# Kernel tuning notes

Measured on AMD Instinct MI355X. Metric: run time of the kernel, lower is better.

## Reference

```python
import jax, jax.numpy as jnp
import numpy as np

# Static config (matches init_kwargs)
VOCAB, EMBED, HIDDEN = 32000, 256, 512
SLOTS, MEM_DIM, HEADS, TOPK = 1024, 64, 4, 8
B, T = 16, 128
# beta_read/beta_write are learned scalars but the torch forward detaches them
# via .item(); treat as constants (|beta| + 1e-6 with beta init ~1.0).
BETA_R = 1.0 + 1e-6
BETA_W = 1.0 + 1e-6
EPS = 1e-8


def setup_inputs() -> dict:
    key = jax.random.key(0)
    ks = jax.random.split(key, 16)
    s = 0.02
    HD = HEADS * MEM_DIM
    return {
        "input_seq": jax.random.randint(ks[0], (B, T), 0, VOCAB),
        "E": jax.random.normal(ks[1], (VOCAB, EMBED), jnp.float32) * s,
        "W_ih": jax.random.normal(ks[2], (4 * HIDDEN, EMBED + MEM_DIM), jnp.float32) * s,
        "W_hh": jax.random.normal(ks[3], (4 * HIDDEN, HIDDEN), jnp.float32) * s,
        "b_ih": jnp.zeros((4 * HIDDEN,), jnp.float32),
        "b_hh": jnp.zeros((4 * HIDDEN,), jnp.float32),
        "W_out": jax.random.normal(ks[4], (HIDDEN, VOCAB), jnp.float32) * s,
        "b_out": jnp.zeros((VOCAB,), jnp.float32),
        "W_rk": jax.random.normal(ks[5], (HIDDEN, HD), jnp.float32) * s,
        "b_rk": jnp.zeros((HD,), jnp.float32),
        "W_wk": jax.random.normal(ks[6], (HIDDEN, HD), jnp.float32) * s,
        "b_wk": jnp.zeros((HD,), jnp.float32),
        "W_wv": jax.random.normal(ks[7], (HIDDEN, HD), jnp.float32) * s,
        "b_wv": jnp.zeros((HD,), jnp.float32),
        "W_er": jax.random.normal(ks[8], (HIDDEN, HD), jnp.float32) * s,
        "b_er": jnp.zeros((HD,), jnp.float32),
    }


def _address(memory, keys, beta):
    # memory: [B,S,D], keys: [B,H,D] -> sparse (top-k) content weights [B,H,S]
    mem_n = memory / (jnp.linalg.norm(memory, axis=-1, keepdims=True) + EPS)
    key_n = keys / (jnp.linalg.norm(keys, axis=-1, keepdims=True) + EPS)
    scores = beta * jnp.einsum("bhd,bsd->bhs", key_n, mem_n)
    vals, idx = jax.lax.top_k(scores, TOPK)           # [B,H,K]
    sm = jax.nn.softmax(vals, axis=-1)                # softmax over top-k only
    w = jnp.zeros_like(scores)
    b_ix = jnp.arange(scores.shape[0])[:, None, None]
    h_ix = jnp.arange(HEADS)[None, :, None]
    return w.at[b_ix, h_ix, idx].set(sm)              # [B,H,S]


def reference(input_seq, E, W_ih, W_hh, b_ih, b_hh, W_out, b_out,
              W_rk, b_rk, W_wk, b_wk, W_wv, b_wv, W_er, b_er):
    Bq = input_seq.shape[0]
    memory0 = jnp.full((Bq, SLOTS, MEM_DIM), 1e-6, jnp.float32)
    h0 = jnp.zeros((Bq, HIDDEN), jnp.float32)
    c0 = jnp.zeros((Bq, HIDDEN), jnp.float32)
    r0 = jnp.zeros((Bq, MEM_DIM), jnp.float32)

    def step(carry, x_t):
        memory, h, c, read_vec = carry
        emb = E[x_t]                                          # [B,embed]
        inp = jnp.concatenate([emb, read_vec], axis=-1)
        gates = inp @ W_ih.T + b_ih + h @ W_hh.T + b_hh       # [B,4H]
        i, f, g, o = jnp.split(gates, 4, axis=-1)             # torch LSTM order
        c = jax.nn.sigmoid(f) * c + jax.nn.sigmoid(i) * jnp.tanh(g)
        h = jax.nn.sigmoid(o) * jnp.tanh(c)
        logits = h @ W_out + b_out                            # [B,V]
        rk = (h @ W_rk + b_rk).reshape(Bq, HEADS, MEM_DIM)
        wk = (h @ W_wk + b_wk).reshape(Bq, HEADS, MEM_DIM)
        wv = (h @ W_wv + b_wv).reshape(Bq, HEADS, MEM_DIM)
        er = jax.nn.sigmoid(h @ W_er + b_er).reshape(Bq, HEADS, MEM_DIM)
        # content-addressed top-k read
        rw = _address(memory, rk, BETA_R)                     # [B,H,S]
        read_vec = jnp.einsum("bhs,bsd->bhd", rw, memory).mean(axis=1)
        # erase + add write
        ww = _address(memory, wk, BETA_W)                     # [B,H,S]
        keep = jnp.prod(1.0 - ww[..., None] * er[:, :, None, :], axis=1)
        add = jnp.einsum("bhs,bhd->bsd", ww, wv)
        memory = memory * keep + add
        return (memory, h, c, read_vec), logits

    _, logits_seq = jax.lax.scan(step, (memory0, h0, c0, r0), input_seq.T)
    return jnp.transpose(logits_seq, (1, 0, 2))               # [B,T,V]
```

## Files before the change

kernel.cpp:

```cpp
#include <hip/hip_runtime.h>
#include <hip/hip_bf16.h>
#include <stdint.h>

typedef unsigned int uint;
typedef unsigned short ushort;
typedef unsigned long long u64;
typedef __attribute__((ext_vector_type(8))) short s8v;
typedef __attribute__((ext_vector_type(4))) float f4v;

#define T_STEPS 128
#define BQ 16
#define HID 512
#define NSLOT 1024
#define MD 64
#define VOCAB 32000
#define BETA 1.000001f
#define EPSN 1e-8f

#define NWK 128
#define NBT 16

#define LF_FH(b)  ((b)*32)
#define LF_FP(w)  ((16+(w))*32)
#define LF_FC(w)  ((48+(w))*32)
#define LF_FW(b)  ((176+(b))*32)
#define LF_FG(w)  ((192+(w))*32)
#define NLINES    320

#define AL4(dst, p) asm volatile("global_load_dwordx4 %0, %1, off sc0 sc1" : "=v"(dst) : "v"(p))
#define ALF(dst, p) asm volatile("global_load_dword %0, %1, off sc0 sc1" : "=v"(dst) : "v"(p))
#define AWAIT() do { asm volatile("s_waitcnt vmcnt(0)" ::: "memory"); __builtin_amdgcn_sched_barrier(0); } while(0)
#define DRAIN() asm volatile("s_waitcnt vmcnt(0)" ::: "memory")

__device__ __forceinline__ float sigm(float x){ return 1.f/(1.f+expf(-x)); }
__device__ __forceinline__ void astoref(float* p, float v){
  __hip_atomic_store(p, v, __ATOMIC_RELAXED, __HIP_MEMORY_SCOPE_AGENT);
}
__device__ __forceinline__ void astoreu32(uint* p, uint v){
  __hip_atomic_store(p, v, __ATOMIC_RELAXED, __HIP_MEMORY_SCOPE_AGENT);
}
__device__ __forceinline__ void astoreu64(u64* p, u64 v){
  __hip_atomic_store(p, v, __ATOMIC_RELAXED, __HIP_MEMORY_SCOPE_AGENT);
}
__device__ __forceinline__ u64 aloadu64(const u64* p){
  return __hip_atomic_load((u64*)p, __ATOMIC_RELAXED, __HIP_MEMORY_SCOPE_AGENT);
}
__device__ __forceinline__ uint aloadu32(const uint* p){
  return __hip_atomic_load((uint*)p, __ATOMIC_RELAXED, __HIP_MEMORY_SCOPE_AGENT);
}
__device__ __forceinline__ void poll1(const uint* p, uint gen){
  while (aloadu32(p) < gen) __builtin_amdgcn_s_sleep(2);
}

__device__ __forceinline__ u64 packsc(float v, int slot){
  uint u = __float_as_uint(v);
  u = (u & 0x80000000u) ? ~u : (u | 0x80000000u);
  return ((u64)u << 10) | (u64)(1023 - slot);
}
__device__ __forceinline__ float unpackval(u64 p){
  uint u = (uint)(p >> 10);
  uint bits = (u & 0x80000000u) ? (u & 0x7fffffffu) : ~u;
  return __uint_as_float(bits);
}
__device__ __forceinline__ int unpackslot(u64 p){ return 1023 - (int)(p & 1023u); }

__device__ __forceinline__ ushort f2bf(float x){
  __hip_bfloat16 h = __float2bfloat16(x);
  return *(ushort*)&h;
}
__device__ __forceinline__ float bf2f(ushort u){
  __hip_bfloat16 h; *(ushort*)&h = u;
  return __bfloat162float(h);
}

#define L_MEM  0
#define L_NRM  8704
#define L_HS   8832
#define L_KEY  17088
#define L_KNRM 17600
#define L_SC   17608
#define L_WV   18632
#define L_ER   18888
#define L_WL   19144
#define L_TOT  19208

__global__ __launch_bounds__(256) void prep_emb(const float* __restrict__ E,
                                                const int* __restrict__ seq,
                                                float* __restrict__ EMB){
  int m = blockIdx.x, t = m >> 4, b = m & 15;
  int x = seq[b*T_STEPS + t];
  EMB[(size_t)m*256 + threadIdx.x] = E[(size_t)x*256 + threadIdx.x];
}

__global__ __launch_bounds__(256) void gemm_emb(const float* __restrict__ A,
                                                const float* __restrict__ W_ih,
                                                const float* __restrict__ b_ih,
                                                const float* __restrict__ b_hh,
                                                float* __restrict__ C){
  __shared__ __align__(16) float As[16*68];
  __shared__ __align__(16) float Bs[16*68];
  int mt = blockIdx.x & 31, nt = blockIdx.x >> 5;
  int m0 = mt*64, n0 = nt*64;
  int tx = threadIdx.x & 15, ty = threadIdx.x >> 4;
  float acc[4][4] = {};
  for (int k0 = 0; k0 < 256; k0 += 16){
    int mm = threadIdx.x >> 2, kq = (threadIdx.x & 3)*4;
    float4 a = *(const float4*)(A + (size_t)(m0+mm)*256 + k0 + kq);
    As[(kq+0)*68+mm]=a.x; As[(kq+1)*68+mm]=a.y; As[(kq+2)*68+mm]=a.z; As[(kq+3)*68+mm]=a.w;
    int pp = n0 + mm;
    int r = (pp & 3)*512 + (pp >> 2);
    float4 bv = *(const float4*)(W_ih + (size_t)r*320 + k0 + kq);
    Bs[(kq+0)*68+mm]=bv.x; Bs[(kq+1)*68+mm]=bv.y; Bs[(kq+2)*68+mm]=bv.z; Bs[(kq+3)*68+mm]=bv.w;
    __syncthreads();
    #pragma unroll
    for (int kk = 0; kk < 16; ++kk){
      float4 av = *(const float4*)(As + kk*68 + ty*4);
      float4 bb = *(const float4*)(Bs + kk*68 + tx*4);
      float aa[4] = {av.x,av.y,av.z,av.w};
      float bv2[4] = {bb.x,bb.y,bb.z,bb.w};
      #pragma unroll
      for (int i = 0; i < 4; ++i)
        #pragma unroll
        for (int j = 0; j < 4; ++j)
          acc[i][j] = fmaf(aa[i], bv2[j], acc[i][j]);
    }
    __syncthreads();
  }
  #pragma unroll
  for (int i = 0; i < 4; ++i){
    int m = m0 + ty*4 + i;
    #pragma unroll
    for (int j = 0; j < 4; ++j){
      int pp = n0 + tx*4 + j;
      int r = (pp & 3)*512 + (pp >> 2);
      C[(size_t)m*2048 + pp] = acc[i][j] + b_ih[r] + b_hh[r];
    }
  }
}

__global__ __launch_bounds__(256) void make_wrvT(const float* __restrict__ W_ih,
                                                 float* __restrict__ WT){
  int idx = blockIdx.x*256 + threadIdx.x;
  int k = idx >> 11, p = idx & 2047;
  int r = (p & 3)*512 + (p >> 2);
  WT[idx] = W_ih[(size_t)r*320 + 256 + k];
}

__global__ __launch_bounds__(256) void split_BT(const float* __restrict__ W,
                                                ushort* __restrict__ BThi,
                                                ushort* __restrict__ BTlo){
  __shared__ float tl[32][33];
  int kt = blockIdx.x & 15, nt = blockIdx.x >> 4;
  int k0 = kt*32, n0 = nt*32;
  int tx = threadIdx.x & 31, ty = threadIdx.x >> 5;
  #pragma unroll
  for (int i = 0; i < 4; ++i)
    tl[ty + i*8][tx] = W[(size_t)(k0 + ty + i*8)*VOCAB + n0 + tx];
  __syncthreads();
  #pragma unroll
  for (int i = 0; i < 4; ++i){
    float x = tl[tx][ty + i*8];
    ushort hi = f2bf(x);
    ushort lo = f2bf(x - bf2f(hi));
    size_t o = (size_t)(n0 + ty + i*8)*512 + k0 + tx;
    BThi[o] = hi; BTlo[o] = lo;
  }
}

__global__ __launch_bounds__(256) void split_A(const float* __restrict__ H,
                                               ushort* __restrict__ Ahi,
                                               ushort* __restrict__ Alo){
  int idx = blockIdx.x*256 + threadIdx.x;
  float x = H[idx];
  ushort hi = f2bf(x);
  Ahi[idx] = hi;
  Alo[idx] = f2bf(x - bf2f(hi));
}

__global__ __launch_bounds__(256) void recur_kernel(
    const float* __restrict__ W_hh, const float* __restrict__ WT,
    const float* __restrict__ W_rk, const float* __restrict__ b_rk,
    const float* __restrict__ W_wk, const float* __restrict__ b_wk,
    const float* __restrict__ W_wv, const float* __restrict__ b_wv,
    const float* __restrict__ W_er, const float* __restrict__ b_er,
    const float* __restrict__ G_emb, float* __restrict__ H_all,
    float* __restrict__ H_pub, float* __restrict__ mem_g,
    float* __restrict__ projpub, float* __restrict__ gatespub,
    u64* __restrict__ cand, u64* __restrict__ wlist,
    uint* __restrict__ arrv)
{
  __shared__ __align__(16) float smem[L_TOT];
  const int tid = threadIdx.x;
  const int wg  = blockIdx.x;

  if (wg < NWK){
    float* mem_s  = smem + L_MEM;
    float* nrm_s  = smem + L_NRM;
    float* hs     = smem + L_HS;
    float* key_s  = smem + L_KEY;
    float* knrm_s = smem + L_KNRM;
    float* sc_s   = smem + L_SC;
    float* wv_s   = smem + L_WV;
    float* er_s   = smem + L_ER;
    u64*   wl_s   = (u64*)(smem + L_WL);

    const int b_s = wg >> 3, rg = wg & 7, s0 = rg*128;
    const int gb = tid >> 4, gc = tid & 15;
    const int pcol = wg*16 + gc;
    const int rrow = (pcol & 3)*512 + (pcol >> 2);
    float* mslice_g = mem_g + ((size_t)b_s*NSLOT + s0)*MD;
    const float* W1 = (wg < 16) ? W_rk : W_wk;
    const float* B1 = (wg < 16) ? b_rk : b_wk;
    const float* W2 = (wg < 16) ? W_wv : W_er;
    const float* B2 = (wg < 16) ? b_wv : b_er;
    const int cc = (wg & 15)*16 + gc;
    const float pb1 = (wg < 32) ? B1[cc] : 0.f;
    const float pb2 = (wg < 32) ? B2[cc] : 0.f;

    for (int i = tid; i < 128*MD; i += 256){
      mem_s[(i >> 6)*68 + (i & 63)] = 1e-6f;
      astoref(mslice_g + i, 1e-6f);
    }
    __syncthreads();
    {
      int s = tid >> 1, half = tid & 1;
      const float4* mp = (const float4*)(mem_s + s*68 + half*32);
      float sum = 0.f;
      #pragma unroll
      for (int q = 0; q < 8; ++q){
        float4 v = mp[q];
        sum = fmaf(v.x,v.x,sum); sum = fmaf(v.y,v.y,sum);
        sum = fmaf(v.z,v.z,sum); sum = fmaf(v.w,v.w,sum);
      }
      sum += __shfl_xor(sum, 1);
      if (half == 0) nrm_s[s] = sqrtf(sum) + EPSN;
    }
    __syncthreads();

    #pragma clang loop unroll(disable)
    for (int t = 0; t < T_STEPS-1; ++t){
      const int par = t & 1, parp = par ^ 1;
      if (t > 0){
        if (tid == 0) poll1(arrv + LF_FW(b_s), (uint)t);
        __syncthreads();
        if (tid < 32) wl_s[tid] = aloadu64(wlist + (size_t)b_s*32 + tid);
        if (tid < 64){
          float4 v; AL4(v, (const float4*)(projpub + (size_t)parp*BQ*1024 + (size_t)b_s*1024 + 512) + tid);
          AWAIT();
          *(float4*)(wv_s + tid*4) = v;
        } else if (tid < 128){
          int i = tid - 64;
          float4 v; AL4(v, (const float4*)(projpub + (size_t)parp*BQ*1024 + (size_t)b_s*1024 + 768) + i);
          AWAIT();
          *(float4*)(er_s + i*4) = v;
        }
        __syncthreads();
        if (tid < 64){
          const int d = tid;
          #pragma unroll 1
          for (int e = 0; e < 32; ++e){
            u64 w64 = wl_s[e];
            int sl = (int)(w64 & 0xffffffffu);
            if (sl >= s0 && sl < s0+128){
              float w = __uint_as_float((uint)(w64 >> 32));
              mem_s[(sl-s0)*68 + d] *= (1.f - w*er_s[(e >> 3)*64 + d]);
            }
          }
          #pragma unroll 1
          for (int e = 0; e < 32; ++e){
            u64 w64 = wl_s[e];
            int sl = (int)(w64 & 0xffffffffu);
            if (sl >= s0 && sl < s0+128){
              float w = __uint_as_float((uint)(w64 >> 32));
              mem_s[(sl-s0)*68 + d] += w*wv_s[(e >> 3)*64 + d];
            }
          }
          #pragma unroll 1
          for (int e = 0; e < 32; ++e){
            u64 w64 = wl_s[e];
            int sl = (int)(w64 & 0xffffffffu);
            if (sl >= s0 && sl < s0+128)
              astoref(mslice_g + (sl-s0)*MD + d, mem_s[(sl-s0)*68 + d]);
          }
        }
        __syncthreads();
        {
          int s = tid >> 1, half = tid & 1;
          const float4* mp = (const float4*)(mem_s + s*68 + half*32);
          float sum = 0.f;
          #pragma unroll
          for (int q = 0; q < 8; ++q){
            float4 v = mp[q];
            sum = fmaf(v.x,v.x,sum); sum = fmaf(v.y,v.y,sum);
            sum = fmaf(v.z,v.z,sum); sum = fmaf(v.w,v.w,sum);
          }
          sum += __shfl_xor(sum, 1);
          if (half == 0) nrm_s[s] = sqrtf(sum) + EPSN;
        }
      }
      if (tid < 16) poll1(arrv + LF_FH(tid), (uint)(t+1));
      __syncthreads();
      {
        float4 v0,v1,v2,v3,v4,v5,v6,v7;
        const float4* hp = (const float4*)H_pub;
        AL4(v0, hp + tid);        AL4(v1, hp + tid + 256);
        AL4(v2, hp + tid + 512);  AL4(v3, hp + tid + 768);
        AL4(v4, hp + tid + 1024); AL4(v5, hp + tid + 1280);
        AL4(v6, hp + tid + 1536); AL4(v7, hp + tid + 1792);
        AWAIT();
        int i;
        i = tid;        *(float4*)(hs + (i>>7)*516 + (i&127)*4) = v0;
        i = tid + 256;  *(float4*)(hs + (i>>7)*516 + (i&127)*4) = v1;
        i = tid + 512;  *(float4*)(hs + (i>>7)*516 + (i&127)*4) = v2;
        i = tid + 768;  *(float4*)(hs + (i>>7)*516 + (i&127)*4) = v3;
        i = tid + 1024; *(float4*)(hs + (i>>7)*516 + (i&127)*4) = v4;
        i = tid + 1280; *(float4*)(hs + (i>>7)*516 + (i&127)*4) = v5;
        i = tid + 1536; *(float4*)(hs + (i>>7)*516 + (i&127)*4) = v6;
        i = tid + 1792; *(float4*)(hs + (i>>7)*516 + (i&127)*4) = v7;
      }
      __syncthreads();
      if (wg < 32){
        float a0=0.f,a1=0.f,b0=0.f,b1=0.f;
        const float* hp = hs + gb*516;
        const float* w1 = W1 + cc;
        const float* w2 = W2 + cc;
        #pragma unroll 4
        for (int k = 0; k < 512; k += 2){
          float h0 = hp[k], h1 = hp[k+1];
          a0 = fmaf(h0, w1[(size_t)k*256], a0);
          b0 = fmaf(h0, w2[(size_t)k*256], b0);
          a1 = fmaf(h1, w1[(size_t)(k+1)*256], a1);
          b1 = fmaf(h1, w2[(size_t)(k+1)*256], b1);
        }
        float v1 = a0 + a1 + pb1;
        float v2 = b0 + b1 + pb2;
        if (wg >= 16) v2 = sigm(v2);
        astoref(projpub + (size_t)par*BQ*1024 + (size_t)gb*1024 + wg*16 + gc, v1);
        astoref(projpub + (size_t)par*BQ*1024 + (size_t)gb*1024 + 512 + wg*16 + gc, v2);
      }
      DRAIN();
      __syncthreads();
      if (wg < 32 && tid == 0) astoreu32(arrv + LF_FP(wg), (uint)(t+1));
      if (tid < 32) poll1(arrv + LF_FP(tid), (uint)(t+1));
      __syncthreads();
      if (tid < 128){
        float4 kv; AL4(kv, (const float4*)(projpub + (size_t)par*BQ*1024 + (size_t)b_s*1024) + tid);
        AWAIT();
        *(float4*)(key_s + tid*4) = kv;
      }
      __syncthreads();
      if (tid < 8){
        const float4* kp = (const float4*)(key_s + tid*MD);
        float sum = 0.f;
        #pragma unroll
        for (int q = 0; q < 16; ++q){
          float4 v = kp[q];
          sum = fmaf(v.x,v.x,sum); sum = fmaf(v.y,v.y,sum);
          sum = fmaf(v.z,v.z,sum); sum = fmaf(v.w,v.w,sum);
        }
        knrm_s[tid] = sqrtf(sum) + EPSN;
      }
      __syncthreads();
      {
        int s = tid >> 1, kh = tid & 1;
        const float4* mp = (const float4*)(mem_s + s*68);
        float rnm = 1.f / nrm_s[s];
        float acc4[4] = {0.f,0.f,0.f,0.f};
        #pragma unroll
        for (int q = 0; q < 16; ++q){
          float4 m = mp[q];
          #pragma unroll
          for (int kk = 0; kk < 4; ++kk){
            float4 k4 = *(const float4*)(key_s + (kh*4+kk)*MD + q*4);
            acc4[kk] = fmaf(m.x,k4.x,acc4[kk]); acc4[kk] = fmaf(m.y,k4.y,acc4[kk]);
            acc4[kk] = fmaf(m.z,k4.z,acc4[kk]); acc4[kk] = fmaf(m.w,k4.w,acc4[kk]);
          }
        }
        #pragma unroll
        for (int kk = 0; kk < 4; ++kk){
          int key = kh*4 + kk;
          sc_s[key*128 + s] = BETA * acc4[kk] * rnm / knrm_s[key];
        }
      }
      __syncthreads();
      {
        int wid = tid >> 6, lane = tid & 63;
        #pragma unroll
        for (int kk = 0; kk < 2; ++kk){
          int key = wid*2 + kk;
          u64 p0 = packsc(sc_s[key*128 + lane],      s0 + lane);
          u64 p1 = packsc(sc_s[key*128 + 64 + lane], s0 + 64 + lane);
          #pragma unroll
          for (int r = 0; r < 8; ++r){
            u64 m = p0 > p1 ? p0 : p1;
            #pragma unroll
            for (int o = 32; o; o >>= 1){ u64 q = __shfl_xor(m, o); if (q > m) m = q; }
            if (p0 == m) p0 = 0; else if (p1 == m) p1 = 0;
            if (lane == 0) astoreu64(cand + (((size_t)b_s*8 + key)*8 + rg)*8 + r, m);
          }
        }
      }
      DRAIN();
      __syncthreads();
      if (tid == 0) astoreu32(arrv + LF_FC(wg), (uint)(t+1));
      {
        float a0 = G_emb[(size_t)((t+1)*BQ + gb)*2048 + pcol];
        float a1 = 0.f, a2 = 0.f, a3 = 0.f;
        const float4* wh = (const float4*)(W_hh + (size_t)rrow*HID);
        const float4* xv = (const float4*)(hs + gb*516);
        #pragma unroll 2
        for (int k = 0; k < 128; k += 4){
          float4 w, x;
          w=wh[k+0]; x=xv[k+0]; a0=fmaf(w.x,x.x,a0); a0=fmaf(w.y,x.y,a0); a0=fmaf(w.z,x.z,a0); a0=fmaf(w.w,x.w,a0);
          w=wh[k+1]; x=xv[k+1]; a1=fmaf(w.x,x.x,a1); a1=fmaf(w.y,x.y,a1); a1=fmaf(w.z,x.z,a1); a1=fmaf(w.w,x.w,a1);
          w=wh[k+2]; x=xv[k+2]; a2=fmaf(w.x,x.x,a2); a2=fmaf(w.y,x.y,a2); a2=fmaf(w.z,x.z,a2); a2=fmaf(w.w,x.w,a2);
          w=wh[k+3]; x=xv[k+3]; a3=fmaf(w.x,x.x,a3); a3=fmaf(w.y,x.y,a3); a3=fmaf(w.z,x.z,a3); a3=fmaf(w.w,x.w,a3);
        }
        astoref(gatespub + (size_t)gb*2048 + pcol, (a0+a1)+(a2+a3));
      }
      DRAIN();
      __syncthreads();
      if (tid == 0) astoreu32(arrv + LF_FG(wg), (uint)(t+1));
    }
  } else {
    const int b = wg - NWK;
    float* rv_st = smem;
    float* rv_s  = smem + 256;
    float* gl    = smem + 320;
    float c0, c1;
    {
      float4 gA = *(const float4*)(G_emb + (size_t)b*2048 + tid*8);
      float4 gB = *(const float4*)(G_emb + (size_t)b*2048 + tid*8 + 4);
      c0 = sigm(gA.x)*tanhf(gA.z);
      float h0v = sigm(gA.w)*tanhf(c0);
      c1 = sigm(gB.x)*tanhf(gB.z);
      float h1v = sigm(gB.w)*tanhf(c1);
      astoref(H_pub + (size_t)b*HID + tid*2,     h0v);
      astoref(H_pub + (size_t)b*HID + tid*2 + 1, h1v);
      H_all[(size_t)b*HID + tid*2]     = h0v;
      H_all[(size_t)b*HID + tid*2 + 1] = h1v;
    }
    DRAIN();
    __syncthreads();
    if (tid == 0) astoreu32(arrv + LF_FH(b), 1u);

    #pragma clang loop unroll(disable)
    for (int t = 0; t < T_STEPS-1; ++t){
      if (tid < 8) poll1(arrv + LF_FC(b*8 + tid), (uint)(t+1));
      __syncthreads();
      {
        int wid = tid >> 6, lane = tid & 63;
        #pragma unroll
        for (int kk = 0; kk < 2; ++kk){
          int key = wid*2 + kk;
          u64 pv = aloadu64(cand + (((size_t)b*8 + key)*8 + (lane >> 3))*8 + (lane & 7));
          u64 sel = 0;
          #pragma unroll
          for (int r = 0; r < 8; ++r){
            u64 m = pv;
            #pragma unroll
            for (int o = 32; o; o >>= 1){ u64 q = __shfl_xor(m, o); if (q > m) m = q; }
            if (pv == m) pv = 0;
            if (lane == r) sel = m;
          }
          float val = unpackval(sel);
          int slot = unpackslot(sel);
          float vmax = __shfl(val, 0);
          float e = (lane < 8) ? expf(val - vmax) : 0.f;
          float ssum = e;
          #pragma unroll
          for (int o = 32; o; o >>= 1) ssum += __shfl_xor(ssum, o);
          float w = e / ssum;
          if (key < 4){
            int sls[8];
            #pragma unroll
            for (int i = 0; i < 8; ++i) sls[i] = __shfl(slot, i);
            float mv[8];
            #pragma unroll
            for (int i = 0; i < 8; ++i)
              ALF(mv[i], mem_g + ((size_t)b*NSLOT + sls[i])*MD + lane);
            AWAIT();
            float acc = 0.f;
            #pragma unroll
            for (int i = 0; i < 8; ++i) acc = fmaf(__shfl(w, i), mv[i], acc);
            rv_st[key*64 + lane] = acc;
          } else if (lane < 8){
            astoreu64(wlist + (size_t)b*32 + (key-4)*8 + lane,
                      ((u64)__float_as_uint(w) << 32) | (u64)(uint)slot);
          }
        }
      }
      DRAIN();
      __syncthreads();
      if (tid < 64)
        rv_s[tid] = 0.25f*(rv_st[tid] + rv_st[64+tid] + rv_st[128+tid] + rv_st[192+tid]);
      if (tid == 0) astoreu32(arrv + LF_FW(b), (uint)(t+1));
      if (tid < 128) poll1(arrv + LF_FG(tid), (uint)(t+1));
      __syncthreads();
      {
        float g8[8];
        #pragma unroll
        for (int q = 0; q < 8; ++q)
          ALF(g8[q], gatespub + (size_t)b*2048 + tid + 256*q);
        AWAIT();
        #pragma unroll 2
        for (int d = 0; d < 64; ++d){
          float r = rv_s[d];
          const float* wrow = WT + (size_t)d*2048 + tid;
          #pragma unroll
          for (int q = 0; q < 8; ++q)
            g8[q] = fmaf(r, wrow[256*q], g8[q]);
        }
        #pragma unroll
        for (int q = 0; q < 8; ++q) gl[tid + 256*q] = g8[q];
      }
      __syncthreads();
      {
        float gi0 = gl[tid*8+0], gf0 = gl[tid*8+1], gg0 = gl[tid*8+2], go0 = gl[tid*8+3];
        float gi1 = gl[tid*8+4], gf1 = gl[tid*8+5], gg1 = gl[tid*8+6], go1 = gl[tid*8+7];
        c0 = sigm(gf0)*c0 + sigm(gi0)*tanhf(gg0);
        float h0v = sigm(go0)*tanhf(c0);
        c1 = sigm(gf1)*c1 + sigm(gi1)*tanhf(gg1);
        float h1v = sigm(go1)*tanhf(c1);
        astoref(H_pub + (size_t)b*HID + tid*2,     h0v);
        astoref(H_pub + (size_t)b*HID + tid*2 + 1, h1v);
        H_all[(size_t)((t+1)*BQ + b)*HID + tid*2]     = h0v;
        H_all[(size_t)((t+1)*BQ + b)*HID + tid*2 + 1] = h1v;
      }
      DRAIN();
      __syncthreads();
      if (tid == 0) astoreu32(arrv + LF_FH(b), (uint)(t+2));
    }
  }
}

#define GM_NT 250
__global__ __launch_bounds__(256) void gemm_mfma(
    const ushort* __restrict__ Ahi, const ushort* __restrict__ Alo,
    const ushort* __restrict__ BThi, const ushort* __restrict__ BTlo,
    const float* __restrict__ bias, float* __restrict__ C)
{
  __shared__ __align__(16) ushort ldsu[4*128*40];
  const int tid = threadIdx.x;
  int mt = blockIdx.x / GM_NT, nt = blockIdx.x - mt*GM_NT;
  int m0 = mt*128, n0 = nt*128;
  const int wv = tid >> 6, lane = tid & 63;
  const int wm = (wv & 1)*64, wn = (wv >> 1)*64;
  const int fr = lane & 15, kh = (lane >> 4)*8;

  f4v acc[4][4];
  #pragma unroll
  for (int i = 0; i < 4; ++i)
    #pragma unroll
    for (int j = 0; j < 4; ++j)
      acc[i][j] = (f4v){0.f,0.f,0.f,0.f};

  const int sr = tid & 127, sel = tid >> 7;
  const ushort* srcA = (sel ? Alo : Ahi) + (size_t)(m0 + sr)*512;
  const ushort* srcB = (sel ? BTlo : BThi) + (size_t)(n0 + sr)*512;
  ushort* dstA = ldsu + (size_t)sel*5120 + sr*40;
  ushort* dstB = ldsu + (size_t)(2+sel)*5120 + sr*40;

  for (int ks = 0; ks < 16; ++ks){
    const int k0 = ks*32;
    __syncthreads();
    {
      uint4 a0 = *(const uint4*)(srcA + k0);
      uint4 a1 = *(const uint4*)(srcA + k0 + 8);
      uint4 a2 = *(const uint4*)(srcA + k0 + 16);
      uint4 a3 = *(const uint4*)(srcA + k0 + 24);
      uint4 b0 = *(const uint4*)(srcB + k0);
      uint4 b1 = *(const uint4*)(srcB + k0 + 8);
      uint4 b2 = *(const uint4*)(srcB + k0 + 16);
      uint4 b3 = *(const uint4*)(srcB + k0 + 24);
      *(uint4*)(dstA +  0) = a0; *(uint4*)(dstA +  8) = a1;
      *(uint4*)(dstA + 16) = a2; *(uint4*)(dstA + 24) = a3;
      *(uint4*)(dstB +  0) = b0; *(uint4*)(dstB +  8) = b1;
      *(uint4*)(dstB + 16) = b2; *(uint4*)(dstB + 24) = b3;
    }
    __syncthreads();
    s8v ah[4], al[4], bh[4], bl[4];
    #pragma unroll
    for (int mi = 0; mi < 4; ++mi){
      ah[mi] = *(const s8v*)(ldsu + 0*5120 + (wm + mi*16 + fr)*40 + kh);
      al[mi] = *(const s8v*)(ldsu + 1*5120 + (wm + mi*16 + fr)*40 + kh);
    }
    #pragma unroll
    for (int ni = 0; ni < 4; ++ni){
      bh[ni] = *(const s8v*)(ldsu + 2*5120 + (wn + ni*16 + fr)*40 + kh);
      bl[ni] = *(const s8v*)(ldsu + 3*5120 + (wn + ni*16 + fr)*40 + kh);
    }
    #pragma unroll
    for (int mi = 0; mi < 4; ++mi)
      #pragma unroll
      for (int ni = 0; ni < 4; ++ni){
        acc[mi][ni] = __builtin_amdgcn_mfma_f32_16x16x32_bf16(ah[mi], bh[ni], acc[mi][ni], 0, 0, 0);
        acc[mi][ni] = __builtin_amdgcn_mfma_f32_16x16x32_bf16(ah[mi], bl[ni], acc[mi][ni], 0, 0, 0);
        acc[mi][ni] = __builtin_amdgcn_mfma_f32_16x16x32_bf16(al[mi], bh[ni], acc[mi][ni], 0, 0, 0);
        acc[mi][ni] = __builtin_amdgcn_mfma_f32_16x16x32_bf16(al[mi], bl[ni], acc[mi][ni], 0, 0, 0);
      }
  }
  #pragma unroll
  for (int ni = 0; ni < 4; ++ni){
    int col = n0 + wn + ni*16 + fr;
    float bz = bias[col];
    #pragma unroll
    for (int mi = 0; mi < 4; ++mi){
      #pragma unroll
      for (int j = 0; j < 4; ++j){
        int row = m0 + wm + mi*16 + (lane >> 4)*4 + j;
        C[((size_t)(row & 15)*T_STEPS + (row >> 4))*VOCAB + col] = acc[mi][ni][j] + bz;
      }
    }
  }
}

__global__ __launch_bounds__(256) void gemm_out(const float* __restrict__ A,
                                                const float* __restrict__ Bmat,
                                                const float* __restrict__ bias,
                                                float* __restrict__ C){
  __shared__ __align__(16) float As[16*132];
  __shared__ __align__(16) float Bs[16*64];
  int mt = blockIdx.x & 15, nt = blockIdx.x >> 4;
  int m0 = mt*128, n0 = nt*64;
  int tx = threadIdx.x & 15, ty = threadIdx.x >> 4;
  float acc[8][4] = {};
  for (int k0 = 0; k0 < 512; k0 += 16){
    int mm = threadIdx.x >> 1, kq = (threadIdx.x & 1)*8;
    float4 a0 = *(const float4*)(A + (size_t)(m0+mm)*512 + k0 + kq);
    float4 a1 = *(const float4*)(A + (size_t)(m0+mm)*512 + k0 + kq + 4);
    As[(kq+0)*132+mm]=a0.x; As[(kq+1)*132+mm]=a0.y; As[(kq+2)*132+mm]=a0.z; As[(kq+3)*132+mm]=a0.w;
    As[(kq+4)*132+mm]=a1.x; As[(kq+5)*132+mm]=a1.y; As[(kq+6)*132+mm]=a1.z; As[(kq+7)*132+mm]=a1.w;
    int kk2 = threadIdx.x >> 4, nq = (threadIdx.x & 15)*4;
    *(float4*)(Bs + kk2*64 + nq) = *(const float4*)(Bmat + (size_t)(k0+kk2)*VOCAB + n0 + nq);
    __syncthreads();
    #pragma unroll
    for (int kk = 0; kk < 16; ++kk){
      float4 x0 = *(const float4*)(As + kk*132 + ty*8);
      float4 x1 = *(const float4*)(As + kk*132 + ty*8 + 4);
      float4 bv = *(const float4*)(Bs + kk*64 + tx*4);
      float aa[8] = {x0.x,x0.y,x0.z,x0.w,x1.x,x1.y,x1.z,x1.w};
      float bb[4] = {bv.x,bv.y,bv.z,bv.w};
      #pragma unroll
      for (int i = 0; i < 8; ++i)
        #pragma unroll
        for (int j = 0; j < 4; ++j)
          acc[i][j] = fmaf(aa[i], bb[j], acc[i][j]);
    }
    __syncthreads();
  }
  #pragma unroll
  for (int i = 0; i < 8; ++i){
    int m = m0 + ty*8 + i;
    int bq = m & 15, tt = m >> 4;
    float* crow = C + ((size_t)bq*T_STEPS + tt)*VOCAB + n0 + tx*4;
    #pragma unroll
    for (int j = 0; j < 4; ++j) crow[j] = acc[i][j] + bias[n0 + tx*4 + j];
  }
}

extern "C" void kernel_launch(void* const* d_in, const int* in_sizes, int n_in,
                              void* d_out, int out_size, void* d_ws, size_t ws_size,
                              hipStream_t stream){
  const int*   seq   = (const int*)d_in[0];
  const float* E     = (const float*)d_in[1];
  const float* W_ih  = (const float*)d_in[2];
  const float* W_hh  = (const float*)d_in[3];
  const float* b_ih  = (const float*)d_in[4];
  const float* b_hh  = (const float*)d_in[5];
  const float* W_out = (const float*)d_in[6];
  const float* b_out = (const float*)d_in[7];
  const float* W_rk  = (const float*)d_in[8];
  const float* b_rk  = (const float*)d_in[9];
  const float* W_wk  = (const float*)d_in[10];
  const float* b_wk  = (const float*)d_in[11];
  const float* W_wv  = (const float*)d_in[12];
  const float* b_wv  = (const float*)d_in[13];
  const float* W_er  = (const float*)d_in[14];
  const float* b_er  = (const float*)d_in[15];
  float* out = (float*)d_out;
  (void)in_sizes; (void)n_in; (void)out_size;

  char* ws = (char*)d_ws;
  size_t off = 0;
  auto alloc = [&](size_t bytes) -> void* {
    off = (off + 255) & ~(size_t)255;
    void* p = ws + off;
    off += bytes;
    return p;
  };
  float* EMB      = (float*)alloc((size_t)2048*256*4);
  float* G_emb    = (float*)alloc((size_t)2048*2048*4);
  float* H_all    = (float*)alloc((size_t)2048*512*4);
  float* H_pub    = (float*)alloc((size_t)16*512*4);
  float* mem_g    = (float*)alloc((size_t)16*1024*64*4);
  float* projpub  = (float*)alloc((size_t)2*16*1024*4);
  float* gatespub = (float*)alloc((size_t)16*2048*4);
  u64*   cand     = (u64*)alloc((size_t)16*8*8*8*8);
  u64*   wlist    = (u64*)alloc((size_t)16*32*8);
  float* WT       = (float*)alloc((size_t)64*2048*4);
  uint*  arrv     = (uint*)alloc((size_t)NLINES*32*4);
  ushort* Ahi  = (ushort*)alloc((size_t)2048*512*2);
  ushort* Alo  = (ushort*)alloc((size_t)2048*512*2);
  ushort* BThi = (ushort*)alloc((size_t)VOCAB*512*2);
  ushort* BTlo = (ushort*)alloc((size_t)VOCAB*512*2);
  const bool use_mfma = (off <= ws_size);

  hipMemsetAsync(arrv, 0, (size_t)NLINES*32*4, stream);
  prep_emb<<<2048, 256, 0, stream>>>(E, seq, EMB);
  gemm_emb<<<1024, 256, 0, stream>>>(EMB, W_ih, b_ih, b_hh, G_emb);
  make_wrvT<<<512, 256, 0, stream>>>(W_ih, WT);
  if (use_mfma)
    split_BT<<<16000, 256, 0, stream>>>(W_out, BThi, BTlo);
  recur_kernel<<<NWK + NBT, 256, 0, stream>>>(
      W_hh, WT, W_rk, b_rk, W_wk, b_wk, W_wv, b_wv, W_er, b_er,
      G_emb, H_all, H_pub, mem_g, projpub, gatespub, cand, wlist, arrv);
  if (use_mfma){
    split_A<<<4096, 256, 0, stream>>>(H_all, Ahi, Alo);
    gemm_mfma<<<16*GM_NT, 256, 0, stream>>>(Ahi, Alo, BThi, BTlo, b_out, out);
  } else {
    gemm_out<<<16*500, 256, 0, stream>>>(H_all, W_out, b_out, out);
  }
}
```

Measured before the change: 6.386 ms.

## Overlap output-projection GEMM with recurrence via extra persistent workgroups

```diff
diff --git a/kernel.cpp b/kernel.cpp
--- a/kernel.cpp
+++ b/kernel.cpp
@@ -19,6 +19,8 @@
 
 #define NWK 128
 #define NBT 16
+#define NGEMM 256
+#define GM_NT 250
 
 #define LF_FH(b)  ((b)*32)
 #define LF_FP(w)  ((16+(w))*32)
@@ -50,6 +52,9 @@
 }
 __device__ __forceinline__ void poll1(const uint* p, uint gen){
   while (aloadu32(p) < gen) __builtin_amdgcn_s_sleep(2);
+}
+__device__ __forceinline__ void poll64(const uint* p, uint gen){
+  while (aloadu32(p) < gen) __builtin_amdgcn_s_sleep(64);
 }
 
 __device__ __forceinline__ u64 packsc(float v, int slot){
@@ -167,16 +172,6 @@
   }
 }
 
-__global__ __launch_bounds__(256) void split_A(const float* __restrict__ H,
-                                               ushort* __restrict__ Ahi,
-                                               ushort* __restrict__ Alo){
-  int idx = blockIdx.x*256 + threadIdx.x;
-  float x = H[idx];
-  ushort hi = f2bf(x);
-  Ahi[idx] = hi;
-  Alo[idx] = f2bf(x - bf2f(hi));
-}
-
 __global__ __launch_bounds__(256) void recur_kernel(
     const float* __restrict__ W_hh, const float* __restrict__ WT,
     const float* __restrict__ W_rk, const float* __restrict__ b_rk,
@@ -187,6 +182,8 @@
     float* __restrict__ H_pub, float* __restrict__ mem_g,
     float* __restrict__ projpub, float* __restrict__ gatespub,
     u64* __restrict__ cand, u64* __restrict__ wlist,
+    const ushort* __restrict__ BThi, const ushort* __restrict__ BTlo,
+    const float* __restrict__ b_out, float* __restrict__ C_out,
     uint* __restrict__ arrv)
 {
   __shared__ __align__(16) float smem[L_TOT];
@@ -422,7 +419,7 @@
       __syncthreads();
       if (tid == 0) astoreu32(arrv + LF_FG(wg), (uint)(t+1));
     }
-  } else {
+  } else if (wg < NWK + NBT){
     const int b = wg - NWK;
     float* rv_st = smem;
     float* rv_s  = smem + 256;
@@ -437,8 +434,8 @@
       float h1v = sigm(gB.w)*tanhf(c1);
       astoref(H_pub + (size_t)b*HID + tid*2,     h0v);
       astoref(H_pub + (size_t)b*HID + tid*2 + 1, h1v);
-      H_all[(size_t)b*HID + tid*2]     = h0v;
-      H_all[(size_t)b*HID + tid*2 + 1] = h1v;
+      astoref(H_all + (size_t)b*HID + tid*2,     h0v);
+      astoref(H_all + (size_t)b*HID + tid*2 + 1, h1v);
     }
     DRAIN();
     __syncthreads();
@@ -524,93 +521,98 @@
         float h1v = sigm(go1)*tanhf(c1);
         astoref(H_pub + (size_t)b*HID + tid*2,     h0v);
         astoref(H_pub + (size_t)b*HID + tid*2 + 1, h1v);
-        H_all[(size_t)((t+1)*BQ + b)*HID + tid*2]     = h0v;
-        H_all[(size_t)((t+1)*BQ + b)*HID + tid*2 + 1] = h1v;
+        astoref(H_all + (size_t)((t+1)*BQ + b)*HID + tid*2,     h0v);
+        astoref(H_all + (size_t)((t+1)*BQ + b)*HID + tid*2 + 1, h1v);
       }
       DRAIN();
       __syncthreads();
       if (tid == 0) astoreu32(arrv + LF_FH(b), (uint)(t+2));
     }
-  }
-}
-
-#define GM_NT 250
-__global__ __launch_bounds__(256) void gemm_mfma(
-    const ushort* __restrict__ Ahi, const ushort* __restrict__ Alo,
-    const ushort* __restrict__ BThi, const ushort* __restrict__ BTlo,
-    const float* __restrict__ bias, float* __restrict__ C)
-{
-  __shared__ __align__(16) ushort ldsu[4*128*40];
-  const int tid = threadIdx.x;
-  int mt = blockIdx.x / GM_NT, nt = blockIdx.x - mt*GM_NT;
-  int m0 = mt*128, n0 = nt*128;
-  const int wv = tid >> 6, lane = tid & 63;
-  const int wm = (wv & 1)*64, wn = (wv >> 1)*64;
-  const int fr = lane & 15, kh = (lane >> 4)*8;
-
-  f4v acc[4][4];
-  #pragma unroll
-  for (int i = 0; i < 4; ++i)
-    #pragma unroll
-    for (int j = 0; j < 4; ++j)
-      acc[i][j] = (f4v){0.f,0.f,0.f,0.f};
-
-  const int sr = tid & 127, sel = tid >> 7;
-  const ushort* srcA = (sel ? Alo : Ahi) + (size_t)(m0 + sr)*512;
-  const ushort* srcB = (sel ? BTlo : BThi) + (size_t)(n0 + sr)*512;
-  ushort* dstA = ldsu + (size_t)sel*5120 + sr*40;
-  ushort* dstB = ldsu + (size_t)(2+sel)*5120 + sr*40;
-
-  for (int ks = 0; ks < 16; ++ks){
-    const int k0 = ks*32;
-    __syncthreads();
-    {
-      uint4 a0 = *(const uint4*)(srcA + k0);
-      uint4 a1 = *(const uint4*)(srcA + k0 + 8);
-      uint4 a2 = *(const uint4*)(srcA + k0 + 16);
-      uint4 a3 = *(const uint4*)(srcA + k0 + 24);
-      uint4 b0 = *(const uint4*)(srcB + k0);
-      uint4 b1 = *(const uint4*)(srcB + k0 + 8);
-      uint4 b2 = *(const uint4*)(srcB + k0 + 16);
-      uint4 b3 = *(const uint4*)(srcB + k0 + 24);
-      *(uint4*)(dstA +  0) = a0; *(uint4*)(dstA +  8) = a1;
-      *(uint4*)(dstA + 16) = a2; *(uint4*)(dstA + 24) = a3;
-      *(uint4*)(dstB +  0) = b0; *(uint4*)(dstB +  8) = b1;
-      *(uint4*)(dstB + 16) = b2; *(uint4*)(dstB + 24) = b3;
-    }
-    __syncthreads();
-    s8v ah[4], al[4], bh[4], bl[4];
-    #pragma unroll
-    for (int mi = 0; mi < 4; ++mi){
-      ah[mi] = *(const s8v*)(ldsu + 0*5120 + (wm + mi*16 + fr)*40 + kh);
-      al[mi] = *(const s8v*)(ldsu + 1*5120 + (wm + mi*16 + fr)*40 + kh);
-    }
-    #pragma unroll
-    for (int ni = 0; ni < 4; ++ni){
-      bh[ni] = *(const s8v*)(ldsu + 2*5120 + (wn + ni*16 + fr)*40 + kh);
-      bl[ni] = *(const s8v*)(ldsu + 3*5120 + (wn + ni*16 + fr)*40 + kh);
-    }
-    #pragma unroll
-    for (int mi = 0; mi < 4; ++mi)
+  } else {
+    const int g = wg - (NWK + NBT);
+    ushort* ldsu = (ushort*)smem;
+    const int wv_ = tid >> 6, lane = tid & 63;
+    const int wm = (wv_ & 1)*64, wn = (wv_ >> 1)*64;
+    const int fr = lane & 15, kh = (lane >> 4)*8;
+    const int ar = tid >> 1, ahalf = tid & 1;
+    const int sr = tid & 127, selb = tid >> 7;
+
+    for (int tile = g; tile < 16*GM_NT; tile += NGEMM){
+      int mt = tile / GM_NT, nt = tile - mt*GM_NT;
+      int m0 = mt*128, n0 = nt*128;
+      uint need = (uint)(mt*8 + 8);
+      if (tid < 16) poll64(arrv + LF_FH(tid), need);
+      __syncthreads();
+      f4v acc[4][4];
+      #pragma unroll
+      for (int i = 0; i < 4; ++i)
+        #pragma unroll
+        for (int j = 0; j < 4; ++j)
+          acc[i][j] = (f4v){0.f,0.f,0.f,0.f};
+      const float* srcA = H_all + (size_t)(m0 + ar)*512 + ahalf*16;
+      const ushort* srcB = (selb ? BTlo : BThi) + (size_t)(n0 + sr)*512;
+      ushort* dstAh = ldsu + 0*5120 + ar*40 + ahalf*16;
+      ushort* dstAl = ldsu + 1*5120 + ar*40 + ahalf*16;
+      ushort* dstB  = ldsu + (size_t)(2+selb)*5120 + sr*40;
+      for (int ks = 0; ks < 16; ++ks){
+        const int k0 = ks*32;
+        __syncthreads();
+        float4 fa0, fa1, fa2, fa3;
+        AL4(fa0, (const float4*)(srcA + k0));
+        AL4(fa1, (const float4*)(srcA + k0 + 4));
+        AL4(fa2, (const float4*)(srcA + k0 + 8));
+        AL4(fa3, (const float4*)(srcA + k0 + 12));
+        uint4 b0 = *(const uint4*)(srcB + k0);
+        uint4 b1 = *(const uint4*)(srcB + k0 + 8);
+        uint4 b2 = *(const uint4*)(srcB + k0 + 16);
+        uint4 b3 = *(const uint4*)(srcB + k0 + 24);
+        AWAIT();
+        float fa[16] = {fa0.x,fa0.y,fa0.z,fa0.w, fa1.x,fa1.y,fa1.z,fa1.w,
+                        fa2.x,fa2.y,fa2.z,fa2.w, fa3.x,fa3.y,fa3.z,fa3.w};
+        #pragma unroll
+        for (int j = 0; j < 16; ++j){
+          ushort hi = f2bf(fa[j]);
+          dstAh[j] = hi;
+          dstAl[j] = f2bf(fa[j] - bf2f(hi));
+        }
+        *(uint4*)(dstB +  0) = b0; *(uint4*)(dstB +  8) = b1;
+        *(uint4*)(dstB + 16) = b2; *(uint4*)(dstB + 24) = b3;
+        __syncthreads();
+        s8v ah[4], al[4], bh[4], bl[4];
+        #pragma unroll
+        for (int mi = 0; mi < 4; ++mi){
+          ah[mi] = *(const s8v*)(ldsu + 0*5120 + (wm + mi*16 + fr)*40 + kh);
+          al[mi] = *(const s8v*)(ldsu + 1*5120 + (wm + mi*16 + fr)*40 + kh);
+        }
+        #pragma unroll
+        for (int ni = 0; ni < 4; ++ni){
+          bh[ni] = *(const s8v*)(ldsu + 2*5120 + (wn + ni*16 + fr)*40 + kh);
+          bl[ni] = *(const s8v*)(ldsu + 3*5120 + (wn + ni*16 + fr)*40 + kh);
+        }
+        #pragma unroll
+        for (int mi = 0; mi < 4; ++mi)
+          #pragma unroll
+          for (int ni = 0; ni < 4; ++ni){
+            acc[mi][ni] = __builtin_amdgcn_mfma_f32_16x16x32_bf16(ah[mi], bh[ni], acc[mi][ni], 0, 0, 0);
+            acc[mi][ni] = __builtin_amdgcn_mfma_f32_16x16x32_bf16(ah[mi], bl[ni], acc[mi][ni], 0, 0, 0);
+            acc[mi][ni] = __builtin_amdgcn_mfma_f32_16x16x32_bf16(al[mi], bh[ni], acc[mi][ni], 0, 0, 0);
+            acc[mi][ni] = __builtin_amdgcn_mfma_f32_16x16x32_bf16(al[mi], bl[ni], acc[mi][ni], 0, 0, 0);
+          }
+      }
       #pragma unroll
       for (int ni = 0; ni < 4; ++ni){
-        acc[mi][ni] = __builtin_amdgcn_mfma_f32_16x16x32_bf16(ah[mi], bh[ni], acc[mi][ni], 0, 0, 0);
-        acc[mi][ni] = __builtin_amdgcn_mfma_f32_16x16x32_bf16(ah[mi], bl[ni], acc[mi][ni], 0, 0, 0);
-        acc[mi][ni] = __builtin_amdgcn_mfma_f32_16x16x32_bf16(al[mi], bh[ni], acc[mi][ni], 0, 0, 0);
-        acc[mi][ni] = __builtin_amdgcn_mfma_f32_16x16x32_bf16(al[mi], bl[ni], acc[mi][ni], 0, 0, 0);
-      }
-  }
-  #pragma unroll
-  for (int ni = 0; ni < 4; ++ni){
-    int col = n0 + wn + ni*16 + fr;
-    float bz = bias[col];
-    #pragma unroll
-    for (int mi = 0; mi < 4; ++mi){
-      #pragma unroll
-      for (int j = 0; j < 4; ++j){
-        int row = m0 + wm + mi*16 + (lane >> 4)*4 + j;
-        C[((size_t)(row & 15)*T_STEPS + (row >> 4))*VOCAB + col] = acc[mi][ni][j] + bz;
-      }
+        int col = n0 + wn + ni*16 + fr;
+        float bz = b_out[col];
+        #pragma unroll
+        for (int mi = 0; mi < 4; ++mi){
+          #pragma unroll
+          for (int j = 0; j < 4; ++j){
+            int row = m0 + wm + mi*16 + (lane >> 4)*4 + j;
+            C_out[((size_t)(row & 15)*T_STEPS + (row >> 4))*VOCAB + col] = acc[mi][ni][j] + bz;
+          }
+        }
+      }
+      __syncthreads();
     }
   }
 }
@@ -700,8 +702,6 @@
   u64*   wlist    = (u64*)alloc((size_t)16*32*8);
   float* WT       = (float*)alloc((size_t)64*2048*4);
   uint*  arrv     = (uint*)alloc((size_t)NLINES*32*4);
-  ushort* Ahi  = (ushort*)alloc((size_t)2048*512*2);
-  ushort* Alo  = (ushort*)alloc((size_t)2048*512*2);
   ushort* BThi = (ushort*)alloc((size_t)VOCAB*512*2);
   ushort* BTlo = (ushort*)alloc((size_t)VOCAB*512*2);
   const bool use_mfma = (off <= ws_size);
@@ -712,13 +712,11 @@
   make_wrvT<<<512, 256, 0, stream>>>(W_ih, WT);
   if (use_mfma)
     split_BT<<<16000, 256, 0, stream>>>(W_out, BThi, BTlo);
-  recur_kernel<<<NWK + NBT, 256, 0, stream>>>(
+  int grid = NWK + NBT + (use_mfma ? NGEMM : 0);
+  recur_kernel<<<grid, 256, 0, stream>>>(
       W_hh, WT, W_rk, b_rk, W_wk, b_wk, W_wv, b_wv, W_er, b_er,
-      G_emb, H_all, H_pub, mem_g, projpub, gatespub, cand, wlist, arrv);
-  if (use_mfma){
-    split_A<<<4096, 256, 0, stream>>>(H_all, Ahi, Alo);
-    gemm_mfma<<<16*GM_NT, 256, 0, stream>>>(Ahi, Alo, BThi, BTlo, b_out, out);
-  } else {
+      G_emb, H_all, H_pub, mem_g, projpub, gatespub, cand, wlist,
+      BThi, BTlo, b_out, out, arrv);
+  if (!use_mfma)
     gemm_out<<<16*500, 256, 0, stream>>>(H_all, W_out, b_out, out);
-  }
-}
+}
```

Result: slower. 6.664 ms (+4.4%).
